# Kernel optimization log

Hardware: AMD Instinct MI355X
Metric: run time of the kernel (lower is better)

Reference implementation:

```python
import jax, jax.numpy as jnp
import numpy as np

B, H, N, F, P, NODE = 64, 168, 512, 8, 24, 0


def _lstm(x, k, rk, b, return_sequences):
    # x: (B, T, Fin); keras LSTM gate order i, f, g(c), o
    Bx = x.shape[0]
    U = rk.shape[0]
    h0 = jnp.zeros((Bx, U), x.dtype)

    def step(carry, xt):
        h, c = carry
        z = xt @ k + h @ rk + b
        i, f, g, o = jnp.split(z, 4, axis=-1)
        c = jax.nn.sigmoid(f) * c + jax.nn.sigmoid(i) * jnp.tanh(g)
        h = jax.nn.sigmoid(o) * jnp.tanh(c)
        return (h, c), h

    (_, _), hs = jax.lax.scan(step, (h0, h0), jnp.swapaxes(x, 0, 1))
    return jnp.swapaxes(hs, 0, 1) if return_sequences else hs[-1]


def _node_summaries(inputs):
    # inputs: (B, H, N, F). Per-(b,n) temporal stats over H of feature 0.
    x0 = inputs[..., 0]                      # (B, H, N)
    mean_full = x0.mean(axis=1)              # (B, N)
    mean_half = x0[:, H // 2:].mean(axis=1)
    std_full = x0.std(axis=1)                # population std (ddof=0), like tf
    std_half = x0[:, H // 2:].std(axis=1)
    c = x0 - mean_full[:, None, :]
    m2 = (c * c).mean(axis=1)
    m3 = (c ** 3).mean(axis=1)
    m4 = (c ** 4).mean(axis=1)
    skew = jnp.nan_to_num(m3 / m2 ** 1.5)    # scipy.stats.skew (biased)
    kurt = jnp.nan_to_num(m4 / (m2 * m2) - 3.0)  # scipy Fisher kurtosis
    t = jnp.arange(H, dtype=x0.dtype)
    tc = t - t.mean()
    slope = jnp.nan_to_num(jnp.einsum('h,bhn->bn', tc, x0) / (tc * tc).sum())
    return jnp.stack([mean_full, mean_half, std_full, std_half, skew, kurt, slope], axis=2)  # (B, N, 7)


def reference(inputs, adj, w_gcn1, b_gcn1, w_gcn2, b_gcn2, w_conv1, b_conv1,
              w_conv2, b_conv2, k_lstm1, rk_lstm1, b_lstm1, k_lstm2, rk_lstm2,
              b_lstm2, w_out, b_out):
    nf = _node_summaries(inputs)                                   # (B, N, 7)
    # GraphConv: relu(A @ X @ W + b)
    h = jax.nn.relu(jnp.einsum('nm,bmc->bnc', adj, nf @ w_gcn1) + b_gcn1)
    g = jax.nn.relu(jnp.einsum('nm,bmc->bnc', adj, h @ w_gcn2) + b_gcn2)   # (B, N, 16)
    # Conv1D channels_first: channels = N, steps = 16
    dn = ('NCH', 'HIO', 'NCH')
    c1 = jax.lax.conv_general_dilated(g, w_conv1, (1,), 'SAME', dimension_numbers=dn) + b_conv1[None, :, None]  # (B,4,16)
    p = c1.reshape(B, 4, 8, 2).mean(axis=-1)                        # AveragePooling1D(2)  (B,4,8)
    c2 = jax.lax.conv_general_dilated(p, w_conv2, (1,), 'SAME', dimension_numbers=dn) + b_conv2[None, :, None]  # (B,4,8)
    gcn_out = jnp.concatenate([c2.reshape(B, -1), p.reshape(B, -1)], axis=-1)  # skip connection, (B, 64)
    # LSTM stack on the selected node's time series
    seq = inputs[:, :, NODE, :]                                     # (B, H, F)
    l1 = _lstm(seq, k_lstm1, rk_lstm1, b_lstm1, True)
    l2 = _lstm(l1, k_lstm2, rk_lstm2, b_lstm2, False)               # (B, 128)
    out = jnp.concatenate([gcn_out, l2], axis=-1)                   # (B, 192); dropout is identity at inference
    return out @ w_out + b_out                                      # (B, P)


def setup_inputs() -> dict:
    key = jax.random.key(0)
    ks = jax.random.split(key, 16)
    s = 0.05
    return {
        'inputs': jax.random.normal(ks[0], (B, H, N, F), jnp.float32),
        'adj': jax.random.uniform(ks[1], (N, N), jnp.float32) / N,
        'w_gcn1': jax.random.normal(ks[2], (7, 32), jnp.float32) * s,
        'b_gcn1': jnp.zeros((32,), jnp.float32),
        'w_gcn2': jax.random.normal(ks[3], (32, 16), jnp.float32) * s,
        'b_gcn2': jnp.zeros((16,), jnp.float32),
        'w_conv1': jax.random.normal(ks[4], (3, N, 4), jnp.float32) * s,
        'b_conv1': jnp.zeros((4,), jnp.float32),
        'w_conv2': jax.random.normal(ks[5], (3, 4, 4), jnp.float32) * s,
        'b_conv2': jnp.zeros((4,), jnp.float32),
        'k_lstm1': jax.random.normal(ks[6], (F, 512), jnp.float32) * s,
        'rk_lstm1': jax.random.normal(ks[7], (128, 512), jnp.float32) * s,
        'b_lstm1': jnp.zeros((512,), jnp.float32),
        'k_lstm2': jax.random.normal(ks[8], (128, 512), jnp.float32) * s,
        'rk_lstm2': jax.random.normal(ks[9], (128, 512), jnp.float32) * s,
        'b_lstm2': jnp.zeros((512,), jnp.float32),
        'w_out': jax.random.normal(ks[10], (192, P), jnp.float32) * s,
        'b_out': jnp.zeros((P,), jnp.float32),
    }
```

## Files before the change

### kernel.cpp

```cpp
#include <hip/hip_runtime.h>
#include <cstdint>
#include <cstddef>

#define BB 64
#define HH 168
#define NN 512
#define FF 8
#define UL 128
#define GD 512

__device__ __forceinline__ float sigf(float x){ return 1.0f/(1.0f+__expf(-x)); }
__device__ __forceinline__ float tanhfast(float x){ return 1.0f - 2.0f/(1.0f+__expf(2.0f*x)); }

__global__ __launch_bounds__(256) void k_sum(const float* __restrict__ in, float* __restrict__ ps){
  int bid = blockIdx.x;
  int b = bid>>2, nh = (bid>>1)&1, hh = bid&1;
  int n = nh*256 + threadIdx.x;
  int h0 = hh*84;
  const float* p = in + ((size_t)(b*HH + h0)*NN + n)*FF;
  float s1=0.f,s2=0.f,s3=0.f,s4=0.f,st=0.f;
  #pragma unroll 4
  for(int h=0;h<84;++h){
    float x = p[(size_t)h*NN*FF];
    float hc = (float)(h+h0) - 83.5f;
    s1 += x;
    float x2 = x*x;
    s2 += x2;
    s3 += x2*x;
    s4 += x2*x2;
    st += hc*x;
  }
  float* o = ps + ((size_t)((b*NN+n)*2 + hh))*8;
  o[0]=s1; o[1]=s2; o[2]=s3; o[3]=s4; o[4]=st;
}

__global__ __launch_bounds__(256) void k_sumc(const float* __restrict__ ps, float* __restrict__ nf){
  int idx = blockIdx.x*256 + threadIdx.x;
  const float* a = ps + (size_t)idx*16;
  const float* c2 = a + 8;
  float s1 = a[0]+c2[0], s2 = a[1]+c2[1], s3 = a[2]+c2[2], s4 = a[3]+c2[3], st = a[4]+c2[4];
  float s1h = c2[0], s2h = c2[1];
  const float iH = 1.0f/168.0f, iHh = 1.0f/84.0f;
  float mean = s1*iH, meanh = s1h*iHh;
  float ex2 = s2*iH, ex3 = s3*iH, ex4 = s4*iH;
  float m2 = ex2 - mean*mean;
  float m3 = ex3 - 3.0f*mean*ex2 + 2.0f*mean*mean*mean;
  float m4 = ex4 - 4.0f*mean*ex3 + 6.0f*mean*mean*ex2 - 3.0f*mean*mean*mean*mean;
  m2 = fmaxf(m2, 0.0f);
  float stdf = sqrtf(m2);
  float m2h = fmaxf(s2h*iHh - meanh*meanh, 0.0f);
  float stdh = sqrtf(m2h);
  float denom = m2*stdf;
  float skew = denom > 0.0f ? m3/denom : 0.0f;
  float kurt = m2 > 0.0f ? (m4/(m2*m2) - 3.0f) : 0.0f;
  float slope = st * (1.0f/395122.0f);
  float* o = nf + (size_t)idx*7;
  o[0]=mean; o[1]=meanh; o[2]=stdf; o[3]=stdh; o[4]=skew; o[5]=kurt; o[6]=slope;
}

__global__ __launch_bounds__(256) void k_gcn1(const float* __restrict__ nf, const float* __restrict__ adj,
        const float* __restrict__ w1, const float* __restrict__ b1, float* __restrict__ h1){
  __shared__ float t_s[NN*32];
  __shared__ float adj_s[128*68];
  int b = blockIdx.x>>2, n0 = (blockIdx.x&3)*128;
  int tid = threadIdx.x;
  {
    int c = tid&31;
    float w1c[7];
    #pragma unroll
    for(int k=0;k<7;++k) w1c[k] = w1[k*32+c];
    for(int idx=tid; idx<NN*32; idx+=256){
      int m = idx>>5;
      const float* nfp = nf + (size_t)(b*NN+m)*7;
      float acc = 0.f;
      #pragma unroll
      for(int k=0;k<7;++k) acc += nfp[k]*w1c[k];
      t_s[idx] = acc;
    }
  }
  int c2 = tid&15, nl = tid>>4;
  float acc[8][2];
  #pragma unroll
  for(int j=0;j<8;++j){acc[j][0]=0.f;acc[j][1]=0.f;}
  for(int mt=0; mt<8; ++mt){
    __syncthreads();
    for(int idx=tid; idx<128*64; idx+=256){
      int r = idx>>6, cc = idx&63;
      adj_s[r*68+cc] = adj[(size_t)(n0+r)*NN + mt*64 + cc];
    }
    __syncthreads();
    for(int mm=0; mm<64; mm+=4){
      float2 tv[4];
      #pragma unroll
      for(int q=0;q<4;++q) tv[q] = *(const float2*)&t_s[(mt*64+mm+q)*32 + 2*c2];
      #pragma unroll
      for(int j=0;j<8;++j){
        float4 a4 = *(const float4*)&adj_s[(nl+16*j)*68 + mm];
        acc[j][0] += a4.x*tv[0].x + a4.y*tv[1].x + a4.z*tv[2].x + a4.w*tv[3].x;
        acc[j][1] += a4.x*tv[0].y + a4.y*tv[1].y + a4.z*tv[2].y + a4.w*tv[3].y;
      }
    }
  }
  float bb0 = b1[2*c2], bb1 = b1[2*c2+1];
  #pragma unroll
  for(int j=0;j<8;++j){
    int n = n0 + nl + 16*j;
    float2 v;
    v.x = fmaxf(acc[j][0]+bb0, 0.0f);
    v.y = fmaxf(acc[j][1]+bb1, 0.0f);
    *(float2*)&h1[(size_t)(b*NN+n)*32 + 2*c2] = v;
  }
}

__global__ __launch_bounds__(256) void k_gcn2(const float* __restrict__ h1, const float* __restrict__ adj,
        const float* __restrict__ w2, const float* __restrict__ b2, float* __restrict__ g){
  __shared__ float t_s[NN*16];
  __shared__ float adj_s[128*68];
  int b = blockIdx.x>>2, n0 = (blockIdx.x&3)*128;
  int tid = threadIdx.x;
  {
    int jh = tid&7;
    float w2c0[32], w2c1[32];
    #pragma unroll
    for(int c=0;c<32;++c){ w2c0[c] = w2[c*16+2*jh]; w2c1[c] = w2[c*16+2*jh+1]; }
    for(int idx=tid; idx<NN*8; idx+=256){
      int m = idx>>3;
      const float4* hp = (const float4*)(h1 + (size_t)(b*NN+m)*32);
      float a0=0.f, a1=0.f;
      #pragma unroll
      for(int q=0;q<8;++q){
        float4 hv = hp[q];
        a0 += hv.x*w2c0[4*q] + hv.y*w2c0[4*q+1] + hv.z*w2c0[4*q+2] + hv.w*w2c0[4*q+3];
        a1 += hv.x*w2c1[4*q] + hv.y*w2c1[4*q+1] + hv.z*w2c1[4*q+2] + hv.w*w2c1[4*q+3];
      }
      t_s[m*16+2*jh] = a0;
      t_s[m*16+2*jh+1] = a1;
    }
  }
  int j = tid&15, nl = tid>>4;
  float acc[8];
  #pragma unroll
  for(int q=0;q<8;++q) acc[q]=0.f;
  for(int mt=0; mt<8; ++mt){
    __syncthreads();
    for(int idx=tid; idx<128*64; idx+=256){
      int r = idx>>6, cc = idx&63;
      adj_s[r*68+cc] = adj[(size_t)(n0+r)*NN + mt*64 + cc];
    }
    __syncthreads();
    for(int mm=0; mm<64; mm+=4){
      float tv[4];
      #pragma unroll
      for(int q=0;q<4;++q) tv[q] = t_s[(mt*64+mm+q)*16 + j];
      #pragma unroll
      for(int q=0;q<8;++q){
        float4 a4 = *(const float4*)&adj_s[(nl+16*q)*68 + mm];
        acc[q] += a4.x*tv[0] + a4.y*tv[1] + a4.z*tv[2] + a4.w*tv[3];
      }
    }
  }
  float bbj = b2[j];
  #pragma unroll
  for(int q=0;q<8;++q){
    int n = n0 + nl + 16*q;
    g[(size_t)(b*NN+n)*16 + j] = fmaxf(acc[q]+bbj, 0.0f);
  }
}

__global__ __launch_bounds__(256) void k_conv(const float* __restrict__ g, const float* __restrict__ wc1,
        const float* __restrict__ bc1, const float* __restrict__ wc2, const float* __restrict__ bc2,
        float* __restrict__ feat){
  __shared__ float g_s[NN*16];
  __shared__ float w1_s[3*NN*4];
  __shared__ float c1p[4][4][16];
  __shared__ float c1_s[4][16];
  __shared__ float p_s[4][8];
  int b = blockIdx.x, tid = threadIdx.x;
  for(int idx=tid; idx<NN*16; idx+=256) g_s[idx] = g[(size_t)b*NN*16 + idx];
  for(int idx=tid; idx<3*NN*4; idx+=256) w1_s[idx] = wc1[idx];
  __syncthreads();
  {
    int q = tid>>6, p = tid&63, o = p>>4, x = p&15;
    int c0 = q*128;
    float acc = 0.f;
    #pragma unroll
    for(int k=0;k<3;++k){
      int xx = x + k - 1;
      if(xx>=0 && xx<16){
        #pragma unroll 4
        for(int c=c0;c<c0+128;++c) acc += g_s[c*16+xx]*w1_s[(k*NN+c)*4+o];
      }
    }
    c1p[q][o][x] = acc;
  }
  __syncthreads();
  if(tid<64){
    int o = tid>>4, x = tid&15;
    c1_s[o][x] = c1p[0][o][x]+c1p[1][o][x]+c1p[2][o][x]+c1p[3][o][x] + bc1[o];
  }
  __syncthreads();
  if(tid<32){
    int oo = tid>>3, xp = tid&7;
    float pv = 0.5f*(c1_s[oo][2*xp]+c1_s[oo][2*xp+1]);
    p_s[oo][xp] = pv;
    feat[b*192 + 32 + oo*8 + xp] = pv;
  }
  __syncthreads();
  if(tid<32){
    int oo = tid>>3, x2 = tid&7;
    float a2 = bc2[oo];
    #pragma unroll
    for(int k=0;k<3;++k){
      int xx = x2 + k - 1;
      if(xx>=0 && xx<8){
        #pragma unroll
        for(int c=0;c<4;++c) a2 += p_s[c][xx]*wc2[(k*4+c)*4+oo];
      }
    }
    feat[b*192 + oo*8 + x2] = a2;
  }
}

__global__ __launch_bounds__(512,2) void k_lstm1(const float* __restrict__ in, const float* __restrict__ k1,
        const float* __restrict__ rk1, const float* __restrict__ b1, float* __restrict__ l1){
  __shared__ float seq_s[HH*FF];
  __shared__ float h_s2[4*36];
  __shared__ float a_s[GD];
  int b = blockIdx.x, tid = threadIdx.x;
  int q = tid&3, grp = tid>>2;
  bool q0 = (tid&1)!=0, q1 = (tid&2)!=0;
  float4 w4[32];
  {
    const float4* rkp = (const float4*)rk1;
    #pragma unroll
    for(int k=0;k<32;++k) w4[k] = rkp[(size_t)(q*32+k)*(GD/4) + grp];
  }
  float wkx[FF];
  #pragma unroll
  for(int f=0;f<FF;++f) wkx[f] = k1[f*GD+tid];
  float bz = b1[tid];
  for(int idx=tid; idx<HH*FF; idx+=512)
    seq_s[idx] = in[(size_t)(b*HH + (idx>>3))*NN*FF + (idx&7)];
  if(tid<UL) h_s2[(tid>>5)*36 + (tid&31)] = 0.0f;
  float c = 0.0f;
  __syncthreads();
  const float4* hq = (const float4*)&h_s2[q*36];
  #pragma unroll 1
  for(int t=0;t<HH;++t){
    float4 x0 = *(const float4*)&seq_s[t*FF];
    float4 x1 = *(const float4*)&seq_s[t*FF+4];
    float zx = bz + x0.x*wkx[0]+x0.y*wkx[1]+x0.z*wkx[2]+x0.w*wkx[3]
                  + x1.x*wkx[4]+x1.y*wkx[5]+x1.z*wkx[6]+x1.w*wkx[7];
    float p0=0.f,p1=0.f,p2=0.f,p3=0.f;
    #pragma unroll
    for(int j=0;j<8;++j){
      float4 hv = hq[j];
      p0 += hv.x*w4[4*j].x + hv.y*w4[4*j+1].x + hv.z*w4[4*j+2].x + hv.w*w4[4*j+3].x;
      p1 += hv.x*w4[4*j].y + hv.y*w4[4*j+1].y + hv.z*w4[4*j+2].y + hv.w*w4[4*j+3].y;
      p2 += hv.x*w4[4*j].z + hv.y*w4[4*j+1].z + hv.z*w4[4*j+2].z + hv.w*w4[4*j+3].z;
      p3 += hv.x*w4[4*j].w + hv.y*w4[4*j+1].w + hv.z*w4[4*j+2].w + hv.w*w4[4*j+3].w;
    }
    float send0 = q0 ? p0 : p1;
    float send1 = q0 ? p2 : p3;
    float r0 = __shfl_xor(send0, 1);
    float r1 = __shfl_xor(send1, 1);
    float s0 = (q0 ? p1 : p0) + r0;
    float s1 = (q0 ? p3 : p2) + r1;
    float send2 = q1 ? s0 : s1;
    float r2 = __shfl_xor(send2, 2);
    float z = zx + (q1 ? s1 : s0) + r2;
    float act = ((tid>>7)==2) ? tanhfast(z) : sigf(z);
    a_s[tid] = act;
    __syncthreads();
    int u = tid&127;
    float ia=a_s[u], fa=a_s[UL+u], ga=a_s[2*UL+u], oa=a_s[3*UL+u];
    c = fa*c + ia*ga;
    float hn = oa*tanhfast(c);
    if(tid<UL){
      h_s2[(tid>>5)*36 + (tid&31)] = hn;
      l1[((size_t)b*HH + t)*UL + tid] = hn;
    }
    __syncthreads();
  }
}

__global__ __launch_bounds__(256) void k_zin2(const float* __restrict__ l1, const float* __restrict__ k2,
        const float* __restrict__ b2, float* __restrict__ zin){
  __shared__ float l_s[21*UL];
  int b = blockIdx.x>>3, t0 = (blockIdx.x&7)*21;
  int tid = threadIdx.x;
  for(int idx=tid; idx<21*UL; idx+=256)
    l_s[idx] = l1[((size_t)b*HH + t0 + (idx>>7))*UL + (idx&127)];
  __syncthreads();
  float acc0[21], acc1[21];
  #pragma unroll
  for(int q=0;q<21;++q){acc0[q]=0.f;acc1[q]=0.f;}
  for(int j=0;j<UL;j+=4){
    float kv00=k2[j*GD+tid],     kv01=k2[(j+1)*GD+tid],     kv02=k2[(j+2)*GD+tid],     kv03=k2[(j+3)*GD+tid];
    float kv10=k2[j*GD+tid+256], kv11=k2[(j+1)*GD+tid+256], kv12=k2[(j+2)*GD+tid+256], kv13=k2[(j+3)*GD+tid+256];
    #pragma unroll
    for(int q=0;q<21;++q){
      float4 lv = *(const float4*)&l_s[q*UL + j];
      acc0[q] += lv.x*kv00 + lv.y*kv01 + lv.z*kv02 + lv.w*kv03;
      acc1[q] += lv.x*kv10 + lv.y*kv11 + lv.z*kv12 + lv.w*kv13;
    }
  }
  float bb0 = b2[tid], bb1 = b2[tid+256];
  #pragma unroll
  for(int q=0;q<21;++q){
    zin[((size_t)b*HH + t0 + q)*GD + tid]       = acc0[q] + bb0;
    zin[((size_t)b*HH + t0 + q)*GD + tid + 256] = acc1[q] + bb1;
  }
}

__global__ __launch_bounds__(512,2) void k_lstm2(const float* __restrict__ zin, const float* __restrict__ rk2,
        float* __restrict__ feat){
  __shared__ float h_s2[4*36];
  __shared__ float a_s[GD];
  int b = blockIdx.x, tid = threadIdx.x;
  int q = tid&3, grp = tid>>2;
  bool q0 = (tid&1)!=0, q1 = (tid&2)!=0;
  float4 w4[32];
  {
    const float4* rkp = (const float4*)rk2;
    #pragma unroll
    for(int k=0;k<32;++k) w4[k] = rkp[(size_t)(q*32+k)*(GD/4) + grp];
  }
  if(tid<UL) h_s2[(tid>>5)*36 + (tid&31)] = 0.0f;
  float c = 0.0f;
  float zc = zin[((size_t)b*HH)*GD + tid];
  __syncthreads();
  const float4* hq = (const float4*)&h_s2[q*36];
  #pragma unroll 1
  for(int t=0;t<HH;++t){
    float nz = 0.f;
    if(t+1<HH) nz = zin[((size_t)b*HH+t+1)*GD + tid];
    float p0=0.f,p1=0.f,p2=0.f,p3=0.f;
    #pragma unroll
    for(int j=0;j<8;++j){
      float4 hv = hq[j];
      p0 += hv.x*w4[4*j].x + hv.y*w4[4*j+1].x + hv.z*w4[4*j+2].x + hv.w*w4[4*j+3].x;
      p1 += hv.x*w4[4*j].y + hv.y*w4[4*j+1].y + hv.z*w4[4*j+2].y + hv.w*w4[4*j+3].y;
      p2 += hv.x*w4[4*j].z + hv.y*w4[4*j+1].z + hv.z*w4[4*j+2].z + hv.w*w4[4*j+3].z;
      p3 += hv.x*w4[4*j].w + hv.y*w4[4*j+1].w + hv.z*w4[4*j+2].w + hv.w*w4[4*j+3].w;
    }
    float send0 = q0 ? p0 : p1;
    float send1 = q0 ? p2 : p3;
    float r0 = __shfl_xor(send0, 1);
    float r1 = __shfl_xor(send1, 1);
    float s0 = (q0 ? p1 : p0) + r0;
    float s1 = (q0 ? p3 : p2) + r1;
    float send2 = q1 ? s0 : s1;
    float r2 = __shfl_xor(send2, 2);
    float z = zc + (q1 ? s1 : s0) + r2;
    float act = ((tid>>7)==2) ? tanhfast(z) : sigf(z);
    a_s[tid] = act;
    __syncthreads();
    int u = tid&127;
    float ia=a_s[u], fa=a_s[UL+u], ga=a_s[2*UL+u], oa=a_s[3*UL+u];
    c = fa*c + ia*ga;
    float hn = oa*tanhfast(c);
    if(tid<UL){
      h_s2[(tid>>5)*36 + (tid&31)] = hn;
      if(t==HH-1) feat[b*192 + 64 + tid] = hn;
    }
    __syncthreads();
    zc = nz;
  }
}

__global__ __launch_bounds__(256) void k_out(const float* __restrict__ feat, const float* __restrict__ wo,
        const float* __restrict__ bo, float* __restrict__ out){
  int idx = blockIdx.x*256 + threadIdx.x;
  if(idx >= BB*24) return;
  int b = idx/24, p = idx - b*24;
  float a0 = bo[p], a1 = 0.f, a2 = 0.f, a3 = 0.f;
  const float* f = feat + b*192;
  for(int k=0;k<192;k+=4){
    a0 += f[k]*wo[k*24+p];
    a1 += f[k+1]*wo[(k+1)*24+p];
    a2 += f[k+2]*wo[(k+2)*24+p];
    a3 += f[k+3]*wo[(k+3)*24+p];
  }
  out[idx] = (a0+a1)+(a2+a3);
}

extern "C" void kernel_launch(void* const* d_in, const int* in_sizes, int n_in,
                              void* d_out, int out_size, void* d_ws, size_t ws_size,
                              hipStream_t stream){
  const float* inp = (const float*)d_in[0];
  const float* adj = (const float*)d_in[1];
  const float* w1  = (const float*)d_in[2];
  const float* b1  = (const float*)d_in[3];
  const float* w2  = (const float*)d_in[4];
  const float* b2  = (const float*)d_in[5];
  const float* wc1 = (const float*)d_in[6];
  const float* bc1 = (const float*)d_in[7];
  const float* wc2 = (const float*)d_in[8];
  const float* bc2 = (const float*)d_in[9];
  const float* k1  = (const float*)d_in[10];
  const float* rk1 = (const float*)d_in[11];
  const float* bl1 = (const float*)d_in[12];
  const float* k2  = (const float*)d_in[13];
  const float* rk2 = (const float*)d_in[14];
  const float* bl2 = (const float*)d_in[15];
  const float* wo  = (const float*)d_in[16];
  const float* bo  = (const float*)d_in[17];
  float* out = (float*)d_out;
  float* ws = (float*)d_ws;

  float* ps   = ws;
  float* nf   = ps + 524288;
  float* h1   = nf + 229376;
  float* g    = h1 + 1048576;
  float* feat = g  + 524288;
  float* l1   = feat + 12288;
  float* zin  = l1 + 1376256;

  k_sum  <<<dim3(256), dim3(256), 0, stream>>>(inp, ps);
  k_sumc <<<dim3(128), dim3(256), 0, stream>>>(ps, nf);
  k_gcn1 <<<dim3(256), dim3(256), 0, stream>>>(nf, adj, w1, b1, h1);
  k_gcn2 <<<dim3(256), dim3(256), 0, stream>>>(h1, adj, w2, b2, g);
  k_conv <<<dim3(64),  dim3(256), 0, stream>>>(g, wc1, bc1, wc2, bc2, feat);
  k_lstm1<<<dim3(64),  dim3(512), 0, stream>>>(inp, k1, rk1, bl1, l1);
  k_zin2 <<<dim3(512), dim3(256), 0, stream>>>(l1, k2, bl2, zin);
  k_lstm2<<<dim3(64),  dim3(512), 0, stream>>>(zin, rk2, feat);
  k_out  <<<dim3(6),   dim3(256), 0, stream>>>(feat, wo, bo, out);
}
```

Before: 433.5 us.

## Restructure LSTM step: per-thread full dot, wave-local gate exchange, double-buffered h

Both LSTM kernels now assign one gate column per thread, holding all 128 recurrent weights in registers and computing the full dot product, instead of splitting it across 4 lanes and combining with shuffles. Each wave holds all four gates for 16 units, so gates are exchanged with shuffles rather than through shared memory, and the hidden state is double-buffered. This removes one of the two block barriers per timestep and the shared gate buffer. The cost is 128 weight registers per thread and 128-wide broadcast LDS reads of h, which may cause register spills at 512 threads with two blocks per CU. Activations use a fast reciprocal intrinsic with a branch-free sigmoid/tanh formula.

```diff
diff --git a/kernel.cpp b/kernel.cpp
--- a/kernel.cpp
+++ b/kernel.cpp
@@ -11,6 +11,7 @@
 
 __device__ __forceinline__ float sigf(float x){ return 1.0f/(1.0f+__expf(-x)); }
 __device__ __forceinline__ float tanhfast(float x){ return 1.0f - 2.0f/(1.0f+__expf(2.0f*x)); }
+__device__ __forceinline__ float frcp(float x){ return __builtin_amdgcn_rcpf(x); }
 
 __global__ __launch_bounds__(256) void k_sum(const float* __restrict__ in, float* __restrict__ ps){
   int bid = blockIdx.x;
@@ -224,63 +225,62 @@
 __global__ __launch_bounds__(512,2) void k_lstm1(const float* __restrict__ in, const float* __restrict__ k1,
         const float* __restrict__ rk1, const float* __restrict__ b1, float* __restrict__ l1){
   __shared__ float seq_s[HH*FF];
-  __shared__ float h_s2[4*36];
-  __shared__ float a_s[GD];
+  __shared__ float hbuf[2][UL];
   int b = blockIdx.x, tid = threadIdx.x;
-  int q = tid&3, grp = tid>>2;
-  bool q0 = (tid&1)!=0, q1 = (tid&2)!=0;
-  float4 w4[32];
-  {
-    const float4* rkp = (const float4*)rk1;
-    #pragma unroll
-    for(int k=0;k<32;++k) w4[k] = rkp[(size_t)(q*32+k)*(GD/4) + grp];
-  }
+  int w = tid>>6, l = tid&63, gate = l>>4, us = l&15;
+  int u = w*16 + us;
+  int col = gate*128 + u;
+  float wr[UL];
+  #pragma unroll
+  for(int m=0;m<UL;++m) wr[m] = rk1[m*GD + col];
   float wkx[FF];
   #pragma unroll
-  for(int f=0;f<FF;++f) wkx[f] = k1[f*GD+tid];
-  float bz = b1[tid];
+  for(int f=0;f<FF;++f) wkx[f] = k1[f*GD + col];
+  float bz = b1[col];
+  bool isg = (gate==2);
+  float Ac = isg?1.f:0.f, Bc = isg?-2.f:1.f, Sc = isg?2.f:-1.f;
   for(int idx=tid; idx<HH*FF; idx+=512)
     seq_s[idx] = in[(size_t)(b*HH + (idx>>3))*NN*FF + (idx&7)];
-  if(tid<UL) h_s2[(tid>>5)*36 + (tid&31)] = 0.0f;
+  if(tid<UL){ hbuf[0][tid] = 0.0f; }
   float c = 0.0f;
   __syncthreads();
-  const float4* hq = (const float4*)&h_s2[q*36];
+  float* hr = &hbuf[0][0];
+  float* hw = &hbuf[1][0];
   #pragma unroll 1
   for(int t=0;t<HH;++t){
     float4 x0 = *(const float4*)&seq_s[t*FF];
     float4 x1 = *(const float4*)&seq_s[t*FF+4];
-    float zx = bz + x0.x*wkx[0]+x0.y*wkx[1]+x0.z*wkx[2]+x0.w*wkx[3]
-                  + x1.x*wkx[4]+x1.y*wkx[5]+x1.z*wkx[6]+x1.w*wkx[7];
-    float p0=0.f,p1=0.f,p2=0.f,p3=0.f;
-    #pragma unroll
-    for(int j=0;j<8;++j){
-      float4 hv = hq[j];
-      p0 += hv.x*w4[4*j].x + hv.y*w4[4*j+1].x + hv.z*w4[4*j+2].x + hv.w*w4[4*j+3].x;
-      p1 += hv.x*w4[4*j].y + hv.y*w4[4*j+1].y + hv.z*w4[4*j+2].y + hv.w*w4[4*j+3].y;
-      p2 += hv.x*w4[4*j].z + hv.y*w4[4*j+1].z + hv.z*w4[4*j+2].z + hv.w*w4[4*j+3].z;
-      p3 += hv.x*w4[4*j].w + hv.y*w4[4*j+1].w + hv.z*w4[4*j+2].w + hv.w*w4[4*j+3].w;
-    }
-    float send0 = q0 ? p0 : p1;
-    float send1 = q0 ? p2 : p3;
-    float r0 = __shfl_xor(send0, 1);
-    float r1 = __shfl_xor(send1, 1);
-    float s0 = (q0 ? p1 : p0) + r0;
-    float s1 = (q0 ? p3 : p2) + r1;
-    float send2 = q1 ? s0 : s1;
-    float r2 = __shfl_xor(send2, 2);
-    float z = zx + (q1 ? s1 : s0) + r2;
-    float act = ((tid>>7)==2) ? tanhfast(z) : sigf(z);
-    a_s[tid] = act;
-    __syncthreads();
-    int u = tid&127;
-    float ia=a_s[u], fa=a_s[UL+u], ga=a_s[2*UL+u], oa=a_s[3*UL+u];
+    float z0 = bz + x0.x*wkx[0]+x0.y*wkx[1];
+    float z1 = x0.z*wkx[2]+x0.w*wkx[3];
+    float z2 = x1.x*wkx[4]+x1.y*wkx[5];
+    float z3 = x1.z*wkx[6]+x1.w*wkx[7];
+    const float4* h4 = (const float4*)hr;
+    #pragma unroll
+    for(int j=0;j<32;++j){
+      float4 hv = h4[j];
+      z0 += hv.x*wr[4*j];
+      z1 += hv.y*wr[4*j+1];
+      z2 += hv.z*wr[4*j+2];
+      z3 += hv.w*wr[4*j+3];
+    }
+    float z = (z0+z1)+(z2+z3);
+    float act = Ac + Bc*frcp(1.0f + __expf(Sc*z));
+    float r16 = __shfl_xor(act, 16);
+    float r32 = __shfl_xor(act, 32);
+    float r48 = __shfl_xor(r16, 32);
+    float ia = gate==0?act : gate==1?r16 : gate==2?r32 : r48;
+    float fa = gate==0?r16 : gate==1?act : gate==2?r48 : r32;
+    float ga = gate==0?r32 : gate==1?r48 : gate==2?act : r16;
+    float oa = gate==0?r48 : gate==1?r32 : gate==2?r16 : act;
     c = fa*c + ia*ga;
-    float hn = oa*tanhfast(c);
-    if(tid<UL){
-      h_s2[(tid>>5)*36 + (tid&31)] = hn;
-      l1[((size_t)b*HH + t)*UL + tid] = hn;
-    }
-    __syncthreads();
+    float th = 1.0f - 2.0f*frcp(1.0f + __expf(2.0f*c));
+    float hn = oa*th;
+    if(gate==0){
+      hw[u] = hn;
+      l1[((size_t)b*HH + t)*UL + u] = hn;
+    }
+    __syncthreads();
+    float* tmp = hr; hr = hw; hw = tmp;
   }
 }
 
@@ -315,56 +315,54 @@
 
 __global__ __launch_bounds__(512,2) void k_lstm2(const float* __restrict__ zin, const float* __restrict__ rk2,
         float* __restrict__ feat){
-  __shared__ float h_s2[4*36];
-  __shared__ float a_s[GD];
+  __shared__ float hbuf[2][UL];
   int b = blockIdx.x, tid = threadIdx.x;
-  int q = tid&3, grp = tid>>2;
-  bool q0 = (tid&1)!=0, q1 = (tid&2)!=0;
-  float4 w4[32];
-  {
-    const float4* rkp = (const float4*)rk2;
-    #pragma unroll
-    for(int k=0;k<32;++k) w4[k] = rkp[(size_t)(q*32+k)*(GD/4) + grp];
-  }
-  if(tid<UL) h_s2[(tid>>5)*36 + (tid&31)] = 0.0f;
+  int w = tid>>6, l = tid&63, gate = l>>4, us = l&15;
+  int u = w*16 + us;
+  int col = gate*128 + u;
+  float wr[UL];
+  #pragma unroll
+  for(int m=0;m<UL;++m) wr[m] = rk2[m*GD + col];
+  bool isg = (gate==2);
+  float Ac = isg?1.f:0.f, Bc = isg?-2.f:1.f, Sc = isg?2.f:-1.f;
+  if(tid<UL){ hbuf[0][tid] = 0.0f; }
   float c = 0.0f;
-  float zc = zin[((size_t)b*HH)*GD + tid];
-  __syncthreads();
-  const float4* hq = (const float4*)&h_s2[q*36];
+  float zc = zin[((size_t)b*HH)*GD + col];
+  __syncthreads();
+  float* hr = &hbuf[0][0];
+  float* hw = &hbuf[1][0];
   #pragma unroll 1
   for(int t=0;t<HH;++t){
     float nz = 0.f;
-    if(t+1<HH) nz = zin[((size_t)b*HH+t+1)*GD + tid];
-    float p0=0.f,p1=0.f,p2=0.f,p3=0.f;
-    #pragma unroll
-    for(int j=0;j<8;++j){
-      float4 hv = hq[j];
-      p0 += hv.x*w4[4*j].x + hv.y*w4[4*j+1].x + hv.z*w4[4*j+2].x + hv.w*w4[4*j+3].x;
-      p1 += hv.x*w4[4*j].y + hv.y*w4[4*j+1].y + hv.z*w4[4*j+2].y + hv.w*w4[4*j+3].y;
-      p2 += hv.x*w4[4*j].z + hv.y*w4[4*j+1].z + hv.z*w4[4*j+2].z + hv.w*w4[4*j+3].z;
-      p3 += hv.x*w4[4*j].w + hv.y*w4[4*j+1].w + hv.z*w4[4*j+2].w + hv.w*w4[4*j+3].w;
-    }
-    float send0 = q0 ? p0 : p1;
-    float send1 = q0 ? p2 : p3;
-    float r0 = __shfl_xor(send0, 1);
-    float r1 = __shfl_xor(send1, 1);
-    float s0 = (q0 ? p1 : p0) + r0;
-    float s1 = (q0 ? p3 : p2) + r1;
-    float send2 = q1 ? s0 : s1;
-    float r2 = __shfl_xor(send2, 2);
-    float z = zc + (q1 ? s1 : s0) + r2;
-    float act = ((tid>>7)==2) ? tanhfast(z) : sigf(z);
-    a_s[tid] = act;
-    __syncthreads();
-    int u = tid&127;
-    float ia=a_s[u], fa=a_s[UL+u], ga=a_s[2*UL+u], oa=a_s[3*UL+u];
+    if(t+1<HH) nz = zin[((size_t)b*HH+t+1)*GD + col];
+    float z0 = zc, z1 = 0.f, z2 = 0.f, z3 = 0.f;
+    const float4* h4 = (const float4*)hr;
+    #pragma unroll
+    for(int j=0;j<32;++j){
+      float4 hv = h4[j];
+      z0 += hv.x*wr[4*j];
+      z1 += hv.y*wr[4*j+1];
+      z2 += hv.z*wr[4*j+2];
+      z3 += hv.w*wr[4*j+3];
+    }
+    float z = (z0+z1)+(z2+z3);
+    float act = Ac + Bc*frcp(1.0f + __expf(Sc*z));
+    float r16 = __shfl_xor(act, 16);
+    float r32 = __shfl_xor(act, 32);
+    float r48 = __shfl_xor(r16, 32);
+    float ia = gate==0?act : gate==1?r16 : gate==2?r32 : r48;
+    float fa = gate==0?r16 : gate==1?act : gate==2?r48 : r32;
+    float ga = gate==0?r32 : gate==1?r48 : gate==2?act : r16;
+    float oa = gate==0?r48 : gate==1?r32 : gate==2?r16 : act;
     c = fa*c + ia*ga;
-    float hn = oa*tanhfast(c);
-    if(tid<UL){
-      h_s2[(tid>>5)*36 + (tid&31)] = hn;
-      if(t==HH-1) feat[b*192 + 64 + tid] = hn;
-    }
-    __syncthreads();
+    float th = 1.0f - 2.0f*frcp(1.0f + __expf(2.0f*c));
+    float hn = oa*th;
+    if(gate==0){
+      hw[u] = hn;
+      if(t==HH-1) feat[b*192 + 64 + u] = hn;
+    }
+    __syncthreads();
+    float* tmp = hr; hr = hw; hw = tmp;
     zc = nz;
   }
 }
```

After: 520.2 us. 20.0% more time.

## Co-schedule summary/GCN work inside LSTM kernels and keep gate exchange in-wave

Applied to the files above, without the earlier changes.

Merges the temporal-summary reduction into the first LSTM launch and the first graph convolution into the second LSTM launch as extra blocks, so the independent branches fill idle CUs alongside the 64 latency-bound recurrent blocks. The LSTM thread mapping is remapped so the four gates of a unit sit in one wavefront. Gate values are exchanged with lane shuffles instead of a shared-memory round trip and an extra barrier, and the hidden state is double-buffered so each step needs one barrier. It also uses hardware reciprocal for activations and pins weight registers, which risks slight accuracy loss and register pressure.

```diff
diff --git a/kernel.cpp b/kernel.cpp
--- a/kernel.cpp
+++ b/kernel.cpp
@@ -8,30 +8,118 @@
 #define FF 8
 #define UL 128
 #define GD 512
-
-__device__ __forceinline__ float sigf(float x){ return 1.0f/(1.0f+__expf(-x)); }
-__device__ __forceinline__ float tanhfast(float x){ return 1.0f - 2.0f/(1.0f+__expf(2.0f*x)); }
-
-__global__ __launch_bounds__(256) void k_sum(const float* __restrict__ in, float* __restrict__ ps){
-  int bid = blockIdx.x;
-  int b = bid>>2, nh = (bid>>1)&1, hh = bid&1;
-  int n = nh*256 + threadIdx.x;
-  int h0 = hh*84;
-  const float* p = in + ((size_t)(b*HH + h0)*NN + n)*FF;
-  float s1=0.f,s2=0.f,s3=0.f,s4=0.f,st=0.f;
-  #pragma unroll 4
-  for(int h=0;h<84;++h){
-    float x = p[(size_t)h*NN*FF];
-    float hc = (float)(h+h0) - 83.5f;
-    s1 += x;
-    float x2 = x*x;
-    s2 += x2;
-    s3 += x2*x;
-    s4 += x2*x2;
-    st += hc*x;
-  }
-  float* o = ps + ((size_t)((b*NN+n)*2 + hh))*8;
-  o[0]=s1; o[1]=s2; o[2]=s3; o[3]=s4; o[4]=st;
+#define HSTR 36
+
+__device__ __forceinline__ float frcp(float x){ return __builtin_amdgcn_rcpf(x); }
+__device__ __forceinline__ void pin4(float4 &v){
+  asm volatile("" : "+v"(v.x), "+v"(v.y), "+v"(v.z), "+v"(v.w));
+}
+
+__global__ __launch_bounds__(512,2) void k_fusedA(const float* __restrict__ in,
+      const float* __restrict__ k1, const float* __restrict__ rk1, const float* __restrict__ b1,
+      float* __restrict__ l1, float* __restrict__ ps){
+  __shared__ float seq_s[HH*FF];
+  __shared__ float hbuf[2][4*HSTR];
+  int tid = threadIdx.x;
+
+  if(blockIdx.x >= 64){
+    int sb = blockIdx.x - 64;
+    int b = sb>>1, hh = sb&1;
+    int n = tid;
+    int h0 = hh*84;
+    const float* p = in + ((size_t)(b*HH + h0)*NN + n)*FF;
+    float s1=0.f,s2=0.f,s3=0.f,s4=0.f,st=0.f;
+    #pragma unroll 4
+    for(int h=0;h<84;++h){
+      float x = p[(size_t)h*NN*FF];
+      float hc = (float)(h+h0) - 83.5f;
+      s1 += x;
+      float x2 = x*x;
+      s2 += x2;
+      s3 += x2*x;
+      s4 += x2*x2;
+      st += hc*x;
+    }
+    float* o = ps + ((size_t)((b*NN+n)*2 + hh))*8;
+    o[0]=s1; o[1]=s2; o[2]=s3; o[3]=s4; o[4]=st;
+    return;
+  }
+
+  int b = blockIdx.x;
+  int w = tid>>6, l = tid&63;
+  int gate = l>>4;
+  int s = l&15;
+  int u = w*16 + s;
+  int col = gate*128 + u;
+  int q = l&3;
+  int cbase = gate*128 + w*16 + (s>>2)*4;
+  bool q0 = (l&1)!=0, q1 = (l&2)!=0;
+
+  float4 w4[32];
+  {
+    #pragma unroll
+    for(int k=0;k<32;++k)
+      w4[k] = *(const float4*)(rk1 + (size_t)(q*32+k)*GD + cbase);
+    #pragma unroll
+    for(int k=0;k<32;++k) pin4(w4[k]);
+  }
+  float wkx[FF];
+  #pragma unroll
+  for(int f=0;f<FF;++f) wkx[f] = k1[f*GD+col];
+  float bz = b1[col];
+  bool isg = (gate==2);
+  float Ac = isg?1.f:0.f, Bc = isg?-2.f:1.f, Sc = isg?2.f:-1.f;
+
+  for(int idx=tid; idx<HH*FF; idx+=512)
+    seq_s[idx] = in[(size_t)(b*HH + (idx>>3))*NN*FF + (idx&7)];
+  if(tid<UL) hbuf[0][(tid>>5)*HSTR + (tid&31)] = 0.0f;
+  float c = 0.0f;
+  __syncthreads();
+
+  int cur = 0;
+  #pragma unroll 1
+  for(int t=0;t<HH;++t){
+    const float4* hq = (const float4*)&hbuf[cur][q*HSTR];
+    float p0=0.f,p1=0.f,p2=0.f,p3=0.f;
+    #pragma unroll
+    for(int j=0;j<8;++j){
+      float4 hv = hq[j];
+      p0 += hv.x*w4[4*j].x + hv.y*w4[4*j+1].x + hv.z*w4[4*j+2].x + hv.w*w4[4*j+3].x;
+      p1 += hv.x*w4[4*j].y + hv.y*w4[4*j+1].y + hv.z*w4[4*j+2].y + hv.w*w4[4*j+3].y;
+      p2 += hv.x*w4[4*j].z + hv.y*w4[4*j+1].z + hv.z*w4[4*j+2].z + hv.w*w4[4*j+3].z;
+      p3 += hv.x*w4[4*j].w + hv.y*w4[4*j+1].w + hv.z*w4[4*j+2].w + hv.w*w4[4*j+3].w;
+    }
+    float4 x0 = *(const float4*)&seq_s[t*FF];
+    float4 x1 = *(const float4*)&seq_s[t*FF+4];
+    float zx = bz + x0.x*wkx[0]+x0.y*wkx[1]+x0.z*wkx[2]+x0.w*wkx[3]
+                  + x1.x*wkx[4]+x1.y*wkx[5]+x1.z*wkx[6]+x1.w*wkx[7];
+    float send0 = q0 ? p0 : p1;
+    float send1 = q0 ? p2 : p3;
+    float r0 = __shfl_xor(send0, 1);
+    float r1 = __shfl_xor(send1, 1);
+    float s0 = (q0 ? p1 : p0) + r0;
+    float s1v = (q0 ? p3 : p2) + r1;
+    float send2 = q1 ? s0 : s1v;
+    float r2 = __shfl_xor(send2, 2);
+    float z = zx + (q1 ? s1v : s0) + r2;
+    float act = Ac + Bc*frcp(1.0f + __expf(Sc*z));
+    float r16 = __shfl_xor(act, 16);
+    float r32 = __shfl_xor(act, 32);
+    float r48 = __shfl_xor(r16, 32);
+    float ia = gate==0?act : gate==1?r16 : gate==2?r32 : r48;
+    float fa = gate==0?r16 : gate==1?act : gate==2?r48 : r32;
+    float ga = gate==0?r32 : gate==1?r48 : gate==2?act : r16;
+    float oa = gate==0?r48 : gate==1?r32 : gate==2?r16 : act;
+    c = fa*c + ia*ga;
+    float th = 1.0f - 2.0f*frcp(1.0f + __expf(2.0f*c));
+    float hn = oa*th;
+    if(l<16){
+      hbuf[cur^1][(u>>5)*HSTR + (u&31)] = hn;
+      l1[((size_t)b*HH + t)*UL + u] = hn;
+    }
+    __syncthreads();
+    cur ^= 1;
+  }
 }
 
 __global__ __launch_bounds__(256) void k_sumc(const float* __restrict__ ps, float* __restrict__ nf){
@@ -58,57 +146,159 @@
   o[0]=mean; o[1]=meanh; o[2]=stdf; o[3]=stdh; o[4]=skew; o[5]=kurt; o[6]=slope;
 }
 
-__global__ __launch_bounds__(256) void k_gcn1(const float* __restrict__ nf, const float* __restrict__ adj,
-        const float* __restrict__ w1, const float* __restrict__ b1, float* __restrict__ h1){
+__global__ __launch_bounds__(256) void k_zin2(const float* __restrict__ l1, const float* __restrict__ k2,
+        const float* __restrict__ b2, float* __restrict__ zin){
+  __shared__ float l_s[21*UL];
+  int b = blockIdx.x>>3, t0 = (blockIdx.x&7)*21;
+  int tid = threadIdx.x;
+  for(int idx=tid; idx<21*UL; idx+=256)
+    l_s[idx] = l1[((size_t)b*HH + t0 + (idx>>7))*UL + (idx&127)];
+  __syncthreads();
+  float acc0[21], acc1[21];
+  #pragma unroll
+  for(int q=0;q<21;++q){acc0[q]=0.f;acc1[q]=0.f;}
+  for(int j=0;j<UL;j+=4){
+    float kv00=k2[j*GD+tid],     kv01=k2[(j+1)*GD+tid],     kv02=k2[(j+2)*GD+tid],     kv03=k2[(j+3)*GD+tid];
+    float kv10=k2[j*GD+tid+256], kv11=k2[(j+1)*GD+tid+256], kv12=k2[(j+2)*GD+tid+256], kv13=k2[(j+3)*GD+tid+256];
+    #pragma unroll
+    for(int q=0;q<21;++q){
+      float4 lv = *(const float4*)&l_s[q*UL + j];
+      acc0[q] += lv.x*kv00 + lv.y*kv01 + lv.z*kv02 + lv.w*kv03;
+      acc1[q] += lv.x*kv10 + lv.y*kv11 + lv.z*kv12 + lv.w*kv13;
+    }
+  }
+  float bb0 = b2[tid], bb1 = b2[tid+256];
+  #pragma unroll
+  for(int q=0;q<21;++q){
+    zin[((size_t)b*HH + t0 + q)*GD + tid]       = acc0[q] + bb0;
+    zin[((size_t)b*HH + t0 + q)*GD + tid + 256] = acc1[q] + bb1;
+  }
+}
+
+__global__ __launch_bounds__(512,2) void k_fusedB(const float* __restrict__ zin,
+      const float* __restrict__ rk2, float* __restrict__ feat,
+      const float* __restrict__ nf, const float* __restrict__ adj,
+      const float* __restrict__ w1, const float* __restrict__ b1g, float* __restrict__ h1){
   __shared__ float t_s[NN*32];
   __shared__ float adj_s[128*68];
-  int b = blockIdx.x>>2, n0 = (blockIdx.x&3)*128;
+  __shared__ float hbuf[2][4*HSTR];
   int tid = threadIdx.x;
+
+  if(blockIdx.x >= 64){
+    int gid = blockIdx.x - 64;
+    int b = gid>>2, n0 = (gid&3)*128;
+    int c = tid&31, nl = tid>>5;
+    {
+      float w1c[7];
+      #pragma unroll
+      for(int k=0;k<7;++k) w1c[k] = w1[k*32+c];
+      for(int idx=tid; idx<NN*32; idx+=512){
+        int m = idx>>5;
+        const float* nfp = nf + (size_t)(b*NN+m)*7;
+        float acc = 0.f;
+        #pragma unroll
+        for(int k=0;k<7;++k) acc += nfp[k]*w1c[k];
+        t_s[idx] = acc;
+      }
+    }
+    float acc[8];
+    #pragma unroll
+    for(int j=0;j<8;++j) acc[j]=0.f;
+    for(int mt=0; mt<8; ++mt){
+      __syncthreads();
+      for(int idx=tid; idx<128*64; idx+=512){
+        int r = idx>>6, cc = idx&63;
+        adj_s[r*68+cc] = adj[(size_t)(n0+r)*NN + mt*64 + cc];
+      }
+      __syncthreads();
+      for(int mm=0; mm<64; mm+=4){
+        float tv0 = t_s[(mt*64+mm+0)*32 + c];
+        float tv1 = t_s[(mt*64+mm+1)*32 + c];
+        float tv2 = t_s[(mt*64+mm+2)*32 + c];
+        float tv3 = t_s[(mt*64+mm+3)*32 + c];
+        #pragma unroll
+        for(int j=0;j<8;++j){
+          float4 a4 = *(const float4*)&adj_s[(nl+16*j)*68 + mm];
+          acc[j] += a4.x*tv0 + a4.y*tv1 + a4.z*tv2 + a4.w*tv3;
+        }
+      }
+    }
+    float bb = b1g[c];
+    #pragma unroll
+    for(int j=0;j<8;++j){
+      int n = n0 + nl + 16*j;
+      h1[(size_t)(b*NN+n)*32 + c] = fmaxf(acc[j]+bb, 0.0f);
+    }
+    return;
+  }
+
+  int b = blockIdx.x;
+  int w = tid>>6, l = tid&63;
+  int gate = l>>4;
+  int s = l&15;
+  int u = w*16 + s;
+  int col = gate*128 + u;
+  int q = l&3;
+  int cbase = gate*128 + w*16 + (s>>2)*4;
+  bool q0 = (l&1)!=0, q1 = (l&2)!=0;
+
+  float4 w4[32];
   {
-    int c = tid&31;
-    float w1c[7];
-    #pragma unroll
-    for(int k=0;k<7;++k) w1c[k] = w1[k*32+c];
-    for(int idx=tid; idx<NN*32; idx+=256){
-      int m = idx>>5;
-      const float* nfp = nf + (size_t)(b*NN+m)*7;
-      float acc = 0.f;
-      #pragma unroll
-      for(int k=0;k<7;++k) acc += nfp[k]*w1c[k];
-      t_s[idx] = acc;
-    }
-  }
-  int c2 = tid&15, nl = tid>>4;
-  float acc[8][2];
-  #pragma unroll
-  for(int j=0;j<8;++j){acc[j][0]=0.f;acc[j][1]=0.f;}
-  for(int mt=0; mt<8; ++mt){
+    #pragma unroll
+    for(int k=0;k<32;++k)
+      w4[k] = *(const float4*)(rk2 + (size_t)(q*32+k)*GD + cbase);
+    #pragma unroll
+    for(int k=0;k<32;++k) pin4(w4[k]);
+  }
+  bool isg = (gate==2);
+  float Ac = isg?1.f:0.f, Bc = isg?-2.f:1.f, Sc = isg?2.f:-1.f;
+  if(tid<UL) hbuf[0][(tid>>5)*HSTR + (tid&31)] = 0.0f;
+  float c = 0.0f;
+  float zc = zin[((size_t)b*HH)*GD + col];
+  __syncthreads();
+
+  int cur = 0;
+  #pragma unroll 1
+  for(int t=0;t<HH;++t){
+    float nz = 0.f;
+    if(t+1<HH) nz = zin[((size_t)b*HH+t+1)*GD + col];
+    const float4* hq = (const float4*)&hbuf[cur][q*HSTR];
+    float p0=0.f,p1=0.f,p2=0.f,p3=0.f;
+    #pragma unroll
+    for(int j=0;j<8;++j){
+      float4 hv = hq[j];
+      p0 += hv.x*w4[4*j].x + hv.y*w4[4*j+1].x + hv.z*w4[4*j+2].x + hv.w*w4[4*j+3].x;
+      p1 += hv.x*w4[4*j].y + hv.y*w4[4*j+1].y + hv.z*w4[4*j+2].y + hv.w*w4[4*j+3].y;
+      p2 += hv.x*w4[4*j].z + hv.y*w4[4*j+1].z + hv.z*w4[4*j+2].z + hv.w*w4[4*j+3].z;
+      p3 += hv.x*w4[4*j].w + hv.y*w4[4*j+1].w + hv.z*w4[4*j+2].w + hv.w*w4[4*j+3].w;
+    }
+    float send0 = q0 ? p0 : p1;
+    float send1 = q0 ? p2 : p3;
+    float r0 = __shfl_xor(send0, 1);
+    float r1 = __shfl_xor(send1, 1);
+    float s0 = (q0 ? p1 : p0) + r0;
+    float s1v = (q0 ? p3 : p2) + r1;
+    float send2 = q1 ? s0 : s1v;
+    float r2 = __shfl_xor(send2, 2);
+    float z = zc + (q1 ? s1v : s0) + r2;
+    float act = Ac + Bc*frcp(1.0f + __expf(Sc*z));
+    float r16 = __shfl_xor(act, 16);
+    float r32 = __shfl_xor(act, 32);
+    float r48 = __shfl_xor(r16, 32);
+    float ia = gate==0?act : gate==1?r16 : gate==2?r32 : r48;
+    float fa = gate==0?r16 : gate==1?act : gate==2?r48 : r32;
+    float ga = gate==0?r32 : gate==1?r48 : gate==2?act : r16;
+    float oa = gate==0?r48 : gate==1?r32 : gate==2?r16 : act;
+    c = fa*c + ia*ga;
+    float th = 1.0f - 2.0f*frcp(1.0f + __expf(2.0f*c));
+    float hn = oa*th;
+    if(l<16){
+      hbuf[cur^1][(u>>5)*HSTR + (u&31)] = hn;
+      if(t==HH-1) feat[b*192 + 64 + u] = hn;
+    }
     __syncthreads();
-    for(int idx=tid; idx<128*64; idx+=256){
-      int r = idx>>6, cc = idx&63;
-      adj_s[r*68+cc] = adj[(size_t)(n0+r)*NN + mt*64 + cc];
-    }
-    __syncthreads();
-    for(int mm=0; mm<64; mm+=4){
-      float2 tv[4];
-      #pragma unroll
-      for(int q=0;q<4;++q) tv[q] = *(const float2*)&t_s[(mt*64+mm+q)*32 + 2*c2];
-      #pragma unroll
-      for(int j=0;j<8;++j){
-        float4 a4 = *(const float4*)&adj_s[(nl+16*j)*68 + mm];
-        acc[j][0] += a4.x*tv[0].x + a4.y*tv[1].x + a4.z*tv[2].x + a4.w*tv[3].x;
-        acc[j][1] += a4.x*tv[0].y + a4.y*tv[1].y + a4.z*tv[2].y + a4.w*tv[3].y;
-      }
-    }
-  }
-  float bb0 = b1[2*c2], bb1 = b1[2*c2+1];
-  #pragma unroll
-  for(int j=0;j<8;++j){
-    int n = n0 + nl + 16*j;
-    float2 v;
-    v.x = fmaxf(acc[j][0]+bb0, 0.0f);
-    v.y = fmaxf(acc[j][1]+bb1, 0.0f);
-    *(float2*)&h1[(size_t)(b*NN+n)*32 + 2*c2] = v;
+    cur ^= 1;
+    zc = nz;
   }
 }
 
@@ -218,154 +408,6 @@
       }
     }
     feat[b*192 + oo*8 + x2] = a2;
-  }
-}
-
-__global__ __launch_bounds__(512,2) void k_lstm1(const float* __restrict__ in, const float* __restrict__ k1,
-        const float* __restrict__ rk1, const float* __restrict__ b1, float* __restrict__ l1){
-  __shared__ float seq_s[HH*FF];
-  __shared__ float h_s2[4*36];
-  __shared__ float a_s[GD];
-  int b = blockIdx.x, tid = threadIdx.x;
-  int q = tid&3, grp = tid>>2;
-  bool q0 = (tid&1)!=0, q1 = (tid&2)!=0;
-  float4 w4[32];
-  {
-    const float4* rkp = (const float4*)rk1;
-    #pragma unroll
-    for(int k=0;k<32;++k) w4[k] = rkp[(size_t)(q*32+k)*(GD/4) + grp];
-  }
-  float wkx[FF];
-  #pragma unroll
-  for(int f=0;f<FF;++f) wkx[f] = k1[f*GD+tid];
-  float bz = b1[tid];
-  for(int idx=tid; idx<HH*FF; idx+=512)
-    seq_s[idx] = in[(size_t)(b*HH + (idx>>3))*NN*FF + (idx&7)];
-  if(tid<UL) h_s2[(tid>>5)*36 + (tid&31)] = 0.0f;
-  float c = 0.0f;
-  __syncthreads();
-  const float4* hq = (const float4*)&h_s2[q*36];
-  #pragma unroll 1
-  for(int t=0;t<HH;++t){
-    float4 x0 = *(const float4*)&seq_s[t*FF];
-    float4 x1 = *(const float4*)&seq_s[t*FF+4];
-    float zx = bz + x0.x*wkx[0]+x0.y*wkx[1]+x0.z*wkx[2]+x0.w*wkx[3]
-                  + x1.x*wkx[4]+x1.y*wkx[5]+x1.z*wkx[6]+x1.w*wkx[7];
-    float p0=0.f,p1=0.f,p2=0.f,p3=0.f;
-    #pragma unroll
-    for(int j=0;j<8;++j){
-      float4 hv = hq[j];
-      p0 += hv.x*w4[4*j].x + hv.y*w4[4*j+1].x + hv.z*w4[4*j+2].x + hv.w*w4[4*j+3].x;
-      p1 += hv.x*w4[4*j].y + hv.y*w4[4*j+1].y + hv.z*w4[4*j+2].y + hv.w*w4[4*j+3].y;
-      p2 += hv.x*w4[4*j].z + hv.y*w4[4*j+1].z + hv.z*w4[4*j+2].z + hv.w*w4[4*j+3].z;
-      p3 += hv.x*w4[4*j].w + hv.y*w4[4*j+1].w + hv.z*w4[4*j+2].w + hv.w*w4[4*j+3].w;
-    }
-    float send0 = q0 ? p0 : p1;
-    float send1 = q0 ? p2 : p3;
-    float r0 = __shfl_xor(send0, 1);
-    float r1 = __shfl_xor(send1, 1);
-    float s0 = (q0 ? p1 : p0) + r0;
-    float s1 = (q0 ? p3 : p2) + r1;
-    float send2 = q1 ? s0 : s1;
-    float r2 = __shfl_xor(send2, 2);
-    float z = zx + (q1 ? s1 : s0) + r2;
-    float act = ((tid>>7)==2) ? tanhfast(z) : sigf(z);
-    a_s[tid] = act;
-    __syncthreads();
-    int u = tid&127;
-    float ia=a_s[u], fa=a_s[UL+u], ga=a_s[2*UL+u], oa=a_s[3*UL+u];
-    c = fa*c + ia*ga;
-    float hn = oa*tanhfast(c);
-    if(tid<UL){
-      h_s2[(tid>>5)*36 + (tid&31)] = hn;
-      l1[((size_t)b*HH + t)*UL + tid] = hn;
-    }
-    __syncthreads();
-  }
-}
-
-__global__ __launch_bounds__(256) void k_zin2(const float* __restrict__ l1, const float* __restrict__ k2,
-        const float* __restrict__ b2, float* __restrict__ zin){
-  __shared__ float l_s[21*UL];
-  int b = blockIdx.x>>3, t0 = (blockIdx.x&7)*21;
-  int tid = threadIdx.x;
-  for(int idx=tid; idx<21*UL; idx+=256)
-    l_s[idx] = l1[((size_t)b*HH + t0 + (idx>>7))*UL + (idx&127)];
-  __syncthreads();
-  float acc0[21], acc1[21];
-  #pragma unroll
-  for(int q=0;q<21;++q){acc0[q]=0.f;acc1[q]=0.f;}
-  for(int j=0;j<UL;j+=4){
-    float kv00=k2[j*GD+tid],     kv01=k2[(j+1)*GD+tid],     kv02=k2[(j+2)*GD+tid],     kv03=k2[(j+3)*GD+tid];
-    float kv10=k2[j*GD+tid+256], kv11=k2[(j+1)*GD+tid+256], kv12=k2[(j+2)*GD+tid+256], kv13=k2[(j+3)*GD+tid+256];
-    #pragma unroll
-    for(int q=0;q<21;++q){
-      float4 lv = *(const float4*)&l_s[q*UL + j];
-      acc0[q] += lv.x*kv00 + lv.y*kv01 + lv.z*kv02 + lv.w*kv03;
-      acc1[q] += lv.x*kv10 + lv.y*kv11 + lv.z*kv12 + lv.w*kv13;
-    }
-  }
-  float bb0 = b2[tid], bb1 = b2[tid+256];
-  #pragma unroll
-  for(int q=0;q<21;++q){
-    zin[((size_t)b*HH + t0 + q)*GD + tid]       = acc0[q] + bb0;
-    zin[((size_t)b*HH + t0 + q)*GD + tid + 256] = acc1[q] + bb1;
-  }
-}
-
-__global__ __launch_bounds__(512,2) void k_lstm2(const float* __restrict__ zin, const float* __restrict__ rk2,
-        float* __restrict__ feat){
-  __shared__ float h_s2[4*36];
-  __shared__ float a_s[GD];
-  int b = blockIdx.x, tid = threadIdx.x;
-  int q = tid&3, grp = tid>>2;
-  bool q0 = (tid&1)!=0, q1 = (tid&2)!=0;
-  float4 w4[32];
-  {
-    const float4* rkp = (const float4*)rk2;
-    #pragma unroll
-    for(int k=0;k<32;++k) w4[k] = rkp[(size_t)(q*32+k)*(GD/4) + grp];
-  }
-  if(tid<UL) h_s2[(tid>>5)*36 + (tid&31)] = 0.0f;
-  float c = 0.0f;
-  float zc = zin[((size_t)b*HH)*GD + tid];
-  __syncthreads();
-  const float4* hq = (const float4*)&h_s2[q*36];
-  #pragma unroll 1
-  for(int t=0;t<HH;++t){
-    float nz = 0.f;
-    if(t+1<HH) nz = zin[((size_t)b*HH+t+1)*GD + tid];
-    float p0=0.f,p1=0.f,p2=0.f,p3=0.f;
-    #pragma unroll
-    for(int j=0;j<8;++j){
-      float4 hv = hq[j];
-      p0 += hv.x*w4[4*j].x + hv.y*w4[4*j+1].x + hv.z*w4[4*j+2].x + hv.w*w4[4*j+3].x;
-      p1 += hv.x*w4[4*j].y + hv.y*w4[4*j+1].y + hv.z*w4[4*j+2].y + hv.w*w4[4*j+3].y;
-      p2 += hv.x*w4[4*j].z + hv.y*w4[4*j+1].z + hv.z*w4[4*j+2].z + hv.w*w4[4*j+3].z;
-      p3 += hv.x*w4[4*j].w + hv.y*w4[4*j+1].w + hv.z*w4[4*j+2].w + hv.w*w4[4*j+3].w;
-    }
-    float send0 = q0 ? p0 : p1;
-    float send1 = q0 ? p2 : p3;
-    float r0 = __shfl_xor(send0, 1);
-    float r1 = __shfl_xor(send1, 1);
-    float s0 = (q0 ? p1 : p0) + r0;
-    float s1 = (q0 ? p3 : p2) + r1;
-    float send2 = q1 ? s0 : s1;
-    float r2 = __shfl_xor(send2, 2);
-    float z = zc + (q1 ? s1 : s0) + r2;
-    float act = ((tid>>7)==2) ? tanhfast(z) : sigf(z);
-    a_s[tid] = act;
-    __syncthreads();
-    int u = tid&127;
-    float ia=a_s[u], fa=a_s[UL+u], ga=a_s[2*UL+u], oa=a_s[3*UL+u];
-    c = fa*c + ia*ga;
-    float hn = oa*tanhfast(c);
-    if(tid<UL){
-      h_s2[(tid>>5)*36 + (tid&31)] = hn;
-      if(t==HH-1) feat[b*192 + 64 + tid] = hn;
-    }
-    __syncthreads();
-    zc = nz;
   }
 }
 
@@ -417,13 +459,11 @@
   float* l1   = feat + 12288;
   float* zin  = l1 + 1376256;
 
-  k_sum  <<<dim3(256), dim3(256), 0, stream>>>(inp, ps);
-  k_sumc <<<dim3(128), dim3(256), 0, stream>>>(ps, nf);
-  k_gcn1 <<<dim3(256), dim3(256), 0, stream>>>(nf, adj, w1, b1, h1);
-  k_gcn2 <<<dim3(256), dim3(256), 0, stream>>>(h1, adj, w2, b2, g);
-  k_conv <<<dim3(64),  dim3(256), 0, stream>>>(g, wc1, bc1, wc2, bc2, feat);
-  k_lstm1<<<dim3(64),  dim3(512), 0, stream>>>(inp, k1, rk1, bl1, l1);
-  k_zin2 <<<dim3(512), dim3(256), 0, stream>>>(l1, k2, bl2, zin);
-  k_lstm2<<<dim3(64),  dim3(512), 0, stream>>>(zin, rk2, feat);
-  k_out  <<<dim3(6),   dim3(256), 0, stream>>>(feat, wo, bo, out);
-}
+  k_fusedA<<<dim3(192), dim3(512), 0, stream>>>(inp, k1, rk1, bl1, l1, ps);
+  k_sumc  <<<dim3(128), dim3(256), 0, stream>>>(ps, nf);
+  k_zin2  <<<dim3(512), dim3(256), 0, stream>>>(l1, k2, bl2, zin);
+  k_fusedB<<<dim3(320), dim3(512), 0, stream>>>(zin, rk2, feat, nf, adj, w1, b1, h1);
+  k_gcn2  <<<dim3(256), dim3(256), 0, stream>>>(h1, adj, w2, b2, g);
+  k_conv  <<<dim3(64),  dim3(256), 0, stream>>>(g, wc1, bc1, wc2, bc2, feat);
+  k_out   <<<dim3(6),   dim3(256), 0, stream>>>(feat, wo, bo, out);
+}
```

Result: slower. 1.193 ms (+175.3%).
